# Kernel tuning notes

Hardware: AMD Instinct MI355X
Metric: run time of the kernel (lower is better)

## Reference

```python
import math
import jax, jax.numpy as jnp
import numpy as np

B, S, H, O = 16, 2048, 512, 16


def setup_inputs() -> dict:
    key = jax.random.key(0)
    ks = jax.random.split(key, 8)
    ops = jax.random.normal(ks[7], (S, O), dtype=jnp.float32)
    ops = ops.at[:, 0].set(1.0)  # identity operator (frozen ones)
    return {
        "x": jax.random.normal(ks[0], (B, S, H), dtype=jnp.float32),
        "Wv": jax.random.normal(ks[1], (H, H), dtype=jnp.float32) * 0.02,
        "bv": jax.random.normal(ks[2], (H,), dtype=jnp.float32) * 0.02,
        "Wk": jax.random.normal(ks[3], (H, H), dtype=jnp.float32) * 0.02,
        "bk": jax.random.normal(ks[4], (H,), dtype=jnp.float32) * 0.02,
        "Wq_op": jax.random.normal(ks[5], (H, S), dtype=jnp.float32) * 0.02,
        "bq_op": jax.random.normal(ks[6], (H,), dtype=jnp.float32) * 0.02,
        "operators": ops,
    }


def reference(x, Wv, bv, Wk, bk, Wq_op, bq_op, operators):
    # operator_queries[o] = Linear(S->H)(operator_o)  -> [O, H]
    operator_queries = jnp.einsum('so,hs->oh', operators, Wq_op) + bq_op

    values = x @ Wv.T + bv          # [B, S, H]
    keys = x @ Wk.T + bk            # [B, S, H]

    # single shared key-query logits (original computes it twice identically)
    logits = jnp.einsum('bsh,oh->bso', keys, operator_queries) / math.sqrt(H)

    # relevance softmax over sequence positions s
    relevance_weights = jax.nn.softmax(logits, axis=1)  # [B, S, O]

    # per-operator weighted reduce over s, fused: [B, O, H]
    operator_outputs = jnp.einsum('bsh,bso,so->boh', values, relevance_weights, operators)

    # operator-mixing softmax over operators o
    operator_weights = jax.nn.softmax(logits, axis=-1)  # [B, S, O]

    output = jnp.einsum('bso,boh->bsh', operator_weights, operator_outputs)
    return output, operator_queries
```

## Files before the change

### kernel.cpp

```cpp
#include <hip/hip_runtime.h>

#define BB 16
#define SS 2048
#define HH 512
#define ON 16
#define INV_SQRT_H 0.04419417382415922f

#define WKO_OFF 0
#define C_OFF   8192
#define L_OFF   8208
#define TT_OFF  8464
#define G_OFF   8720
#define OO_OFF  139792
#define ZERO_N  270864
#define OQT_OFF 270864
#define LG_OFF  279056
#define WVT_OFF 803344

__global__ __launch_bounds__(256) void k_oq(const float* __restrict__ Wq,
                                            const float* __restrict__ bq,
                                            const float* __restrict__ ops,
                                            float* __restrict__ ws,
                                            float* __restrict__ oq_out) {
  const int h = blockIdx.x;
  const int t = threadIdx.x;
  float4 acc[4];
  #pragma unroll
  for (int m = 0; m < 4; ++m) acc[m] = make_float4(0.f, 0.f, 0.f, 0.f);
  for (int s = t; s < SS; s += 256) {
    float wq = Wq[(size_t)h * SS + s];
    const float4* op4 = reinterpret_cast<const float4*>(ops + (size_t)s * ON);
    #pragma unroll
    for (int m = 0; m < 4; ++m) {
      float4 v = op4[m];
      acc[m].x += wq * v.x; acc[m].y += wq * v.y;
      acc[m].z += wq * v.z; acc[m].w += wq * v.w;
    }
  }
  __shared__ float red[256][ON];
  #pragma unroll
  for (int m = 0; m < 4; ++m) {
    red[t][4*m+0] = acc[m].x; red[t][4*m+1] = acc[m].y;
    red[t][4*m+2] = acc[m].z; red[t][4*m+3] = acc[m].w;
  }
  __syncthreads();
  for (int st = 128; st > 0; st >>= 1) {
    if (t < st) {
      #pragma unroll
      for (int o = 0; o < ON; ++o) red[t][o] += red[t + st][o];
    }
    __syncthreads();
  }
  if (t < ON) {
    float v = red[0][t] + bq[h];
    oq_out[(size_t)t * HH + h] = v;
    ws[OQT_OFF + (size_t)h * ON + t] = v;
  }
}

__global__ __launch_bounds__(256) void k_wko(const float* __restrict__ Wk,
                                             const float* __restrict__ bk,
                                             float* __restrict__ ws) {
  const int o = blockIdx.x;
  const int hc = blockIdx.y;
  const int t = threadIdx.x;
  const float* __restrict__ oqT = ws + OQT_OFF;
  const int h0 = hc * 64;
  float acc0 = 0.f, acc1 = 0.f;
  for (int h = h0; h < h0 + 64; ++h) {
    float q = oqT[(size_t)h * ON + o];
    acc0 += q * Wk[(size_t)h * HH + t];
    acc1 += q * Wk[(size_t)h * HH + t + 256];
  }
  unsafeAtomicAdd(&ws[WKO_OFF + (size_t)o * HH + t], acc0);
  unsafeAtomicAdd(&ws[WKO_OFF + (size_t)o * HH + t + 256], acc1);
  if (t == 0) {
    float cp = 0.f;
    for (int h = h0; h < h0 + 64; ++h) cp += bk[h] * oqT[(size_t)h * ON + o];
    unsafeAtomicAdd(&ws[C_OFF + o], cp);
  }
}

__global__ __launch_bounds__(256) void k_wvt(const float* __restrict__ Wv,
                                             float* __restrict__ ws) {
  __shared__ float tile[32][33];
  const int tx = threadIdx.x, ty = threadIdx.y;
  const int x0 = blockIdx.x * 32, y0 = blockIdx.y * 32;
  #pragma unroll
  for (int j = 0; j < 4; ++j)
    tile[ty + 8 * j][tx] = Wv[(size_t)(y0 + ty + 8 * j) * HH + x0 + tx];
  __syncthreads();
  float* WvT = ws + WVT_OFF;
  #pragma unroll
  for (int j = 0; j < 4; ++j)
    WvT[(size_t)(x0 + ty + 8 * j) * HH + y0 + tx] = tile[tx][ty + 8 * j];
}

__global__ __launch_bounds__(256) void k_main(const float* __restrict__ x,
                                              const float* __restrict__ ops,
                                              float* __restrict__ ws) {
  const int b = blockIdx.x, sc = blockIdx.y, t = threadIdx.x;
  const int sbase = sc * 64;
  const size_t xbase = ((size_t)b * SS + sbase) * HH;

  __shared__ float red[64][17];
  __shared__ float part[3][64][17];
  __shared__ float el[64][ON];

  const int kq = t >> 6, lane = t & 63;
  const int rg = lane >> 2, oq = lane & 3;
  const int k0 = kq * 128;

  float acc[4][4];
  #pragma unroll
  for (int i = 0; i < 4; ++i)
    #pragma unroll
    for (int j = 0; j < 4; ++j) acc[i][j] = 0.f;

  const float4* __restrict__ wko4 = reinterpret_cast<const float4*>(ws + WKO_OFF);
  #pragma unroll 4
  for (int ch = 0; ch < 32; ++ch) {
    const int kk = k0 + ch * 4;
    float4 xr[4], wr[4];
    #pragma unroll
    for (int i = 0; i < 4; ++i)
      xr[i] = *reinterpret_cast<const float4*>(x + xbase + (size_t)(rg + 16 * i) * HH + kk);
    #pragma unroll
    for (int j = 0; j < 4; ++j)
      wr[j] = wko4[(4 * oq + j) * 128 + (kk >> 2)];
    #pragma unroll
    for (int i = 0; i < 4; ++i)
      #pragma unroll
      for (int j = 0; j < 4; ++j)
        acc[i][j] += xr[i].x * wr[j].x + xr[i].y * wr[j].y
                   + xr[i].z * wr[j].z + xr[i].w * wr[j].w;
  }
  if (kq == 0) {
    #pragma unroll
    for (int i = 0; i < 4; ++i)
      #pragma unroll
      for (int j = 0; j < 4; ++j) red[rg + 16 * i][4 * oq + j] = acc[i][j];
  } else {
    #pragma unroll
    for (int i = 0; i < 4; ++i)
      #pragma unroll
      for (int j = 0; j < 4; ++j) part[kq - 1][rg + 16 * i][4 * oq + j] = acc[i][j];
  }
  __syncthreads();

  {
    const int r = t >> 2, o4 = (t & 3) * 4;
    float lgv[4];
    #pragma unroll
    for (int j = 0; j < 4; ++j) {
      const int o = o4 + j;
      float s = red[r][o] + part[0][r][o] + part[1][r][o] + part[2][r][o] + ws[C_OFF + o];
      lgv[j] = s * INV_SQRT_H;
    }
    *reinterpret_cast<float4*>(ws + LG_OFF + ((size_t)b * SS + sbase + r) * ON + o4) =
        make_float4(lgv[0], lgv[1], lgv[2], lgv[3]);
    *reinterpret_cast<float4*>(&el[r][o4]) =
        make_float4(__expf(lgv[0]), __expf(lgv[1]), __expf(lgv[2]), __expf(lgv[3]));
  }
  __syncthreads();

  if (t < ON) {
    float sl = 0.f, st = 0.f;
    for (int r = 0; r < 64; ++r) {
      float e = el[r][t];
      sl += e;
      st += e * ops[(size_t)(sbase + r) * ON + t];
    }
    unsafeAtomicAdd(&ws[L_OFF + b * ON + t], sl);
    unsafeAtomicAdd(&ws[TT_OFF + b * ON + t], st);
  }

  float a0[ON], a1[ON];
  #pragma unroll
  for (int o = 0; o < ON; ++o) { a0[o] = 0.f; a1[o] = 0.f; }
  for (int s = 0; s < 64; ++s) {
    const float xv0 = x[xbase + (size_t)s * HH + t];
    const float xv1 = x[xbase + (size_t)s * HH + t + 256];
    const float4* e4 = reinterpret_cast<const float4*>(&el[s][0]);
    #pragma unroll
    for (int g = 0; g < 4; ++g) {
      float4 e = e4[g];
      a0[4*g+0] += e.x * xv0; a1[4*g+0] += e.x * xv1;
      a0[4*g+1] += e.y * xv0; a1[4*g+1] += e.y * xv1;
      a0[4*g+2] += e.z * xv0; a1[4*g+2] += e.z * xv1;
      a0[4*g+3] += e.w * xv0; a1[4*g+3] += e.w * xv1;
    }
  }
  float* G = ws + G_OFF + (size_t)b * ON * HH;
  #pragma unroll
  for (int o = 0; o < ON; ++o) {
    unsafeAtomicAdd(&G[(size_t)o * HH + t], a0[o]);
    unsafeAtomicAdd(&G[(size_t)o * HH + t + 256], a1[o]);
  }
}

__global__ __launch_bounds__(256) void k_oo(const float* __restrict__ bv,
                                            float* __restrict__ ws) {
  const int b = blockIdx.x, oqi = blockIdx.y, kq = blockIdx.z, t = threadIdx.x;
  const int o0 = oqi * 4, k0 = kq * 128;
  __shared__ float Gs[4][128];
  __shared__ float invLs[4], tts[4];
  if (t < 4) {
    float invL = 1.f / ws[L_OFF + b * ON + o0 + t];
    invLs[t] = invL;
    tts[t] = ws[TT_OFF + b * ON + o0 + t] * invL;
  }
  __syncthreads();
  {
    int idx = t;
    #pragma unroll
    for (int p = 0; p < 2; ++p, idx += 256) {
      int oo = idx >> 7, kk = idx & 127;
      Gs[oo][kk] = ws[G_OFF + ((size_t)b * ON + o0 + oo) * HH + k0 + kk] * invLs[oo];
    }
  }
  __syncthreads();
  const float* __restrict__ WvT = ws + WVT_OFF;
  float acc[4][2];
  #pragma unroll
  for (int o = 0; o < 4; ++o) { acc[o][0] = 0.f; acc[o][1] = 0.f; }
  for (int k = 0; k < 128; ++k) {
    const float w0 = WvT[(size_t)(k0 + k) * HH + t];
    const float w1 = WvT[(size_t)(k0 + k) * HH + t + 256];
    #pragma unroll
    for (int o = 0; o < 4; ++o) {
      const float g = Gs[o][k];
      acc[o][0] += g * w0; acc[o][1] += g * w1;
    }
  }
  float* OOp = ws + OO_OFF + ((size_t)b * ON + o0) * HH;
  #pragma unroll
  for (int o = 0; o < 4; ++o) {
    float add0 = acc[o][0], add1 = acc[o][1];
    if (kq == 0) { add0 += bv[t] * tts[o]; add1 += bv[t + 256] * tts[o]; }
    unsafeAtomicAdd(&OOp[(size_t)o * HH + t], add0);
    unsafeAtomicAdd(&OOp[(size_t)o * HH + t + 256], add1);
  }
}

__global__ __launch_bounds__(256) void k_out(float* __restrict__ ws,
                                             float* __restrict__ out) {
  const int b = blockIdx.x, sc = blockIdx.y, t = threadIdx.x;
  const int rbase = b * SS + sc * 128;
  __shared__ float OOs[ON * HH];
  __shared__ float wl[128 * ON];
  const float4* OO4 = reinterpret_cast<const float4*>(ws + OO_OFF + (size_t)(b * ON) * HH);
  float4* OOs4 = reinterpret_cast<float4*>(OOs);
  #pragma unroll
  for (int j = 0; j < 8; ++j) OOs4[t + 256 * j] = OO4[t + 256 * j];
  if (t < 128) {
    const float4* lg4 = reinterpret_cast<const float4*>(ws + LG_OFF + (size_t)(rbase + t) * ON);
    float l[ON];
    float4 p0 = lg4[0], p1 = lg4[1], p2 = lg4[2], p3 = lg4[3];
    l[0]=p0.x; l[1]=p0.y; l[2]=p0.z; l[3]=p0.w;
    l[4]=p1.x; l[5]=p1.y; l[6]=p1.z; l[7]=p1.w;
    l[8]=p2.x; l[9]=p2.y; l[10]=p2.z; l[11]=p2.w;
    l[12]=p3.x; l[13]=p3.y; l[14]=p3.z; l[15]=p3.w;
    float m = l[0];
    #pragma unroll
    for (int o = 1; o < ON; ++o) m = fmaxf(m, l[o]);
    float sum = 0.f;
    #pragma unroll
    for (int o = 0; o < ON; ++o) { l[o] = __expf(l[o] - m); sum += l[o]; }
    float inv = 1.f / sum;
    #pragma unroll
    for (int o = 0; o < ON; ++o) wl[t * ON + o] = l[o] * inv;
  }
  __syncthreads();
  const int rsub = t >> 7, hq = t & 127;
  float oo[ON][4];
  #pragma unroll
  for (int o = 0; o < ON; ++o)
    #pragma unroll
    for (int j = 0; j < 4; ++j) oo[o][j] = OOs[o * HH + hq + 128 * j];
  const float4* wl4 = reinterpret_cast<const float4*>(wl);
  for (int i = 0; i < 64; ++i) {
    const int r = rsub * 64 + i;
    float4 w0 = wl4[r * 4 + 0], w1 = wl4[r * 4 + 1], w2 = wl4[r * 4 + 2], w3 = wl4[r * 4 + 3];
    float w[ON];
    w[0]=w0.x; w[1]=w0.y; w[2]=w0.z; w[3]=w0.w;
    w[4]=w1.x; w[5]=w1.y; w[6]=w1.z; w[7]=w1.w;
    w[8]=w2.x; w[9]=w2.y; w[10]=w2.z; w[11]=w2.w;
    w[12]=w3.x; w[13]=w3.y; w[14]=w3.z; w[15]=w3.w;
    float* orow = out + (size_t)(rbase + r) * HH + hq;
    #pragma unroll
    for (int j = 0; j < 4; ++j) {
      float v = 0.f;
      #pragma unroll
      for (int o = 0; o < ON; ++o) v += w[o] * oo[o][j];
      orow[128 * j] = v;
    }
  }
}

extern "C" void kernel_launch(void* const* d_in, const int* in_sizes, int n_in,
                              void* d_out, int out_size, void* d_ws, size_t ws_size,
                              hipStream_t stream) {
  const float* x   = (const float*)d_in[0];
  const float* Wv  = (const float*)d_in[1];
  const float* bv  = (const float*)d_in[2];
  const float* Wk  = (const float*)d_in[3];
  const float* bk  = (const float*)d_in[4];
  const float* Wq  = (const float*)d_in[5];
  const float* bq  = (const float*)d_in[6];
  const float* ops = (const float*)d_in[7];
  float* out = (float*)d_out;
  float* ws  = (float*)d_ws;
  float* oq_out = out + (size_t)BB * SS * HH;

  hipMemsetAsync(ws, 0, (size_t)ZERO_N * sizeof(float), stream);

  k_wvt<<<dim3(16, 16), dim3(32, 8), 0, stream>>>(Wv, ws);
  k_oq<<<512, 256, 0, stream>>>(Wq, bq, ops, ws, oq_out);
  k_wko<<<dim3(16, 8), 256, 0, stream>>>(Wk, bk, ws);
  k_main<<<dim3(16, 32), 256, 0, stream>>>(x, ops, ws);
  k_oo<<<dim3(16, 4, 4), 256, 0, stream>>>(bv, ws);
  k_out<<<dim3(16, 16), 256, 0, stream>>>(ws, out);
}
```

Baseline: 207.6 us.

## Halve row tiles, drop Wv transpose kernel, and vectorize output stage

```diff
diff --git a/kernel.cpp b/kernel.cpp
--- a/kernel.cpp
+++ b/kernel.cpp
@@ -11,11 +11,10 @@
 #define L_OFF   8208
 #define TT_OFF  8464
 #define G_OFF   8720
+#define ZERO_N  139792
 #define OO_OFF  139792
-#define ZERO_N  270864
 #define OQT_OFF 270864
 #define LG_OFF  279056
-#define WVT_OFF 803344
 
 __global__ __launch_bounds__(256) void k_oq(const float* __restrict__ Wq,
                                             const float* __restrict__ bq,
@@ -81,39 +80,24 @@
   }
 }
 
-__global__ __launch_bounds__(256) void k_wvt(const float* __restrict__ Wv,
-                                             float* __restrict__ ws) {
-  __shared__ float tile[32][33];
-  const int tx = threadIdx.x, ty = threadIdx.y;
-  const int x0 = blockIdx.x * 32, y0 = blockIdx.y * 32;
-  #pragma unroll
-  for (int j = 0; j < 4; ++j)
-    tile[ty + 8 * j][tx] = Wv[(size_t)(y0 + ty + 8 * j) * HH + x0 + tx];
-  __syncthreads();
-  float* WvT = ws + WVT_OFF;
-  #pragma unroll
-  for (int j = 0; j < 4; ++j)
-    WvT[(size_t)(x0 + ty + 8 * j) * HH + y0 + tx] = tile[tx][ty + 8 * j];
-}
-
 __global__ __launch_bounds__(256) void k_main(const float* __restrict__ x,
                                               const float* __restrict__ ops,
                                               float* __restrict__ ws) {
   const int b = blockIdx.x, sc = blockIdx.y, t = threadIdx.x;
-  const int sbase = sc * 64;
+  const int sbase = sc * 32;
   const size_t xbase = ((size_t)b * SS + sbase) * HH;
 
-  __shared__ float red[64][17];
-  __shared__ float part[3][64][17];
-  __shared__ float el[64][ON];
+  __shared__ float red[32][17];
+  __shared__ float part[3][32][17];
+  __shared__ float el[32][ON];
 
   const int kq = t >> 6, lane = t & 63;
   const int rg = lane >> 2, oq = lane & 3;
   const int k0 = kq * 128;
 
-  float acc[4][4];
-  #pragma unroll
-  for (int i = 0; i < 4; ++i)
+  float acc[2][4];
+  #pragma unroll
+  for (int i = 0; i < 2; ++i)
     #pragma unroll
     for (int j = 0; j < 4; ++j) acc[i][j] = 0.f;
 
@@ -121,15 +105,15 @@
   #pragma unroll 4
   for (int ch = 0; ch < 32; ++ch) {
     const int kk = k0 + ch * 4;
-    float4 xr[4], wr[4];
-    #pragma unroll
-    for (int i = 0; i < 4; ++i)
+    float4 xr[2], wr[4];
+    #pragma unroll
+    for (int i = 0; i < 2; ++i)
       xr[i] = *reinterpret_cast<const float4*>(x + xbase + (size_t)(rg + 16 * i) * HH + kk);
     #pragma unroll
     for (int j = 0; j < 4; ++j)
       wr[j] = wko4[(4 * oq + j) * 128 + (kk >> 2)];
     #pragma unroll
-    for (int i = 0; i < 4; ++i)
+    for (int i = 0; i < 2; ++i)
       #pragma unroll
       for (int j = 0; j < 4; ++j)
         acc[i][j] += xr[i].x * wr[j].x + xr[i].y * wr[j].y
@@ -137,18 +121,18 @@
   }
   if (kq == 0) {
     #pragma unroll
-    for (int i = 0; i < 4; ++i)
+    for (int i = 0; i < 2; ++i)
       #pragma unroll
       for (int j = 0; j < 4; ++j) red[rg + 16 * i][4 * oq + j] = acc[i][j];
   } else {
     #pragma unroll
-    for (int i = 0; i < 4; ++i)
+    for (int i = 0; i < 2; ++i)
       #pragma unroll
       for (int j = 0; j < 4; ++j) part[kq - 1][rg + 16 * i][4 * oq + j] = acc[i][j];
   }
   __syncthreads();
 
-  {
+  if (t < 128) {
     const int r = t >> 2, o4 = (t & 3) * 4;
     float lgv[4];
     #pragma unroll
@@ -166,7 +150,7 @@
 
   if (t < ON) {
     float sl = 0.f, st = 0.f;
-    for (int r = 0; r < 64; ++r) {
+    for (int r = 0; r < 32; ++r) {
       float e = el[r][t];
       sl += e;
       st += e * ops[(size_t)(sbase + r) * ON + t];
@@ -178,7 +162,7 @@
   float a0[ON], a1[ON];
   #pragma unroll
   for (int o = 0; o < ON; ++o) { a0[o] = 0.f; a1[o] = 0.f; }
-  for (int s = 0; s < 64; ++s) {
+  for (int s = 0; s < 32; ++s) {
     const float xv0 = x[xbase + (size_t)s * HH + t];
     const float xv1 = x[xbase + (size_t)s * HH + t + 256];
     const float4* e4 = reinterpret_cast<const float4*>(&el[s][0]);
@@ -199,11 +183,12 @@
   }
 }
 
-__global__ __launch_bounds__(256) void k_oo(const float* __restrict__ bv,
+__global__ __launch_bounds__(256) void k_oo(const float* __restrict__ Wv,
+                                            const float* __restrict__ bv,
                                             float* __restrict__ ws) {
-  const int b = blockIdx.x, oqi = blockIdx.y, kq = blockIdx.z, t = threadIdx.x;
-  const int o0 = oqi * 4, k0 = kq * 128;
-  __shared__ float Gs[4][128];
+  const int b = blockIdx.x, oqi = blockIdx.y, hqi = blockIdx.z, t = threadIdx.x;
+  const int o0 = oqi * 4, h0 = hqi * 128;
+  __shared__ float4 Gs[4][128];
   __shared__ float invLs[4], tts[4];
   if (t < 4) {
     float invL = 1.f / ws[L_OFF + b * ON + o0 + t];
@@ -216,44 +201,43 @@
     #pragma unroll
     for (int p = 0; p < 2; ++p, idx += 256) {
       int oo = idx >> 7, kk = idx & 127;
-      Gs[oo][kk] = ws[G_OFF + ((size_t)b * ON + o0 + oo) * HH + k0 + kk] * invLs[oo];
-    }
-  }
-  __syncthreads();
-  const float* __restrict__ WvT = ws + WVT_OFF;
-  float acc[4][2];
-  #pragma unroll
-  for (int o = 0; o < 4; ++o) { acc[o][0] = 0.f; acc[o][1] = 0.f; }
-  for (int k = 0; k < 128; ++k) {
-    const float w0 = WvT[(size_t)(k0 + k) * HH + t];
-    const float w1 = WvT[(size_t)(k0 + k) * HH + t + 256];
-    #pragma unroll
-    for (int o = 0; o < 4; ++o) {
-      const float g = Gs[o][k];
-      acc[o][0] += g * w0; acc[o][1] += g * w1;
-    }
+      float4 g = reinterpret_cast<const float4*>(
+          ws + G_OFF + ((size_t)b * ON + o0 + oo) * HH)[kk];
+      float sv = invLs[oo];
+      Gs[oo][kk] = make_float4(g.x * sv, g.y * sv, g.z * sv, g.w * sv);
+    }
+  }
+  __syncthreads();
+  const int hh = h0 + (t & 127);
+  const int op = (t >> 7) * 2;
+  const float4* __restrict__ wv4 = reinterpret_cast<const float4*>(Wv + (size_t)hh * HH);
+  float a0 = 0.f, a1 = 0.f;
+  #pragma unroll 4
+  for (int kk = 0; kk < 128; ++kk) {
+    float4 wv = wv4[kk];
+    float4 g0 = Gs[op][kk], g1 = Gs[op + 1][kk];
+    a0 += g0.x * wv.x + g0.y * wv.y + g0.z * wv.z + g0.w * wv.w;
+    a1 += g1.x * wv.x + g1.y * wv.y + g1.z * wv.z + g1.w * wv.w;
   }
   float* OOp = ws + OO_OFF + ((size_t)b * ON + o0) * HH;
-  #pragma unroll
-  for (int o = 0; o < 4; ++o) {
-    float add0 = acc[o][0], add1 = acc[o][1];
-    if (kq == 0) { add0 += bv[t] * tts[o]; add1 += bv[t + 256] * tts[o]; }
-    unsafeAtomicAdd(&OOp[(size_t)o * HH + t], add0);
-    unsafeAtomicAdd(&OOp[(size_t)o * HH + t + 256], add1);
-  }
+  OOp[(size_t)op * HH + hh]       = a0 + bv[hh] * tts[op];
+  OOp[(size_t)(op + 1) * HH + hh] = a1 + bv[hh] * tts[op + 1];
 }
 
 __global__ __launch_bounds__(256) void k_out(float* __restrict__ ws,
                                              float* __restrict__ out) {
   const int b = blockIdx.x, sc = blockIdx.y, t = threadIdx.x;
-  const int rbase = b * SS + sc * 128;
-  __shared__ float OOs[ON * HH];
-  __shared__ float wl[128 * ON];
-  const float4* OO4 = reinterpret_cast<const float4*>(ws + OO_OFF + (size_t)(b * ON) * HH);
-  float4* OOs4 = reinterpret_cast<float4*>(OOs);
-  #pragma unroll
-  for (int j = 0; j < 8; ++j) OOs4[t + 256 * j] = OO4[t + 256 * j];
-  if (t < 128) {
+  const int rbase = b * SS + sc * 32;
+  __shared__ float wl[32 * ON];
+
+  float4 oo4[ON];
+  const float4* __restrict__ OO4 =
+      reinterpret_cast<const float4*>(ws + OO_OFF + (size_t)b * ON * HH);
+  const int hq = t & 127;
+  #pragma unroll
+  for (int o = 0; o < ON; ++o) oo4[o] = OO4[o * 128 + hq];
+
+  if (t < 32) {
     const float4* lg4 = reinterpret_cast<const float4*>(ws + LG_OFF + (size_t)(rbase + t) * ON);
     float l[ON];
     float4 p0 = lg4[0], p1 = lg4[1], p2 = lg4[2], p3 = lg4[3];
@@ -272,29 +256,25 @@
     for (int o = 0; o < ON; ++o) wl[t * ON + o] = l[o] * inv;
   }
   __syncthreads();
-  const int rsub = t >> 7, hq = t & 127;
-  float oo[ON][4];
-  #pragma unroll
-  for (int o = 0; o < ON; ++o)
-    #pragma unroll
-    for (int j = 0; j < 4; ++j) oo[o][j] = OOs[o * HH + hq + 128 * j];
+
+  const int rsub = t >> 7;
   const float4* wl4 = reinterpret_cast<const float4*>(wl);
-  for (int i = 0; i < 64; ++i) {
-    const int r = rsub * 64 + i;
+  float4* __restrict__ out4 = reinterpret_cast<float4*>(out);
+  for (int i = 0; i < 16; ++i) {
+    const int r = rsub * 16 + i;
     float4 w0 = wl4[r * 4 + 0], w1 = wl4[r * 4 + 1], w2 = wl4[r * 4 + 2], w3 = wl4[r * 4 + 3];
     float w[ON];
     w[0]=w0.x; w[1]=w0.y; w[2]=w0.z; w[3]=w0.w;
     w[4]=w1.x; w[5]=w1.y; w[6]=w1.z; w[7]=w1.w;
     w[8]=w2.x; w[9]=w2.y; w[10]=w2.z; w[11]=w2.w;
     w[12]=w3.x; w[13]=w3.y; w[14]=w3.z; w[15]=w3.w;
-    float* orow = out + (size_t)(rbase + r) * HH + hq;
-    #pragma unroll
-    for (int j = 0; j < 4; ++j) {
-      float v = 0.f;
-      #pragma unroll
-      for (int o = 0; o < ON; ++o) v += w[o] * oo[o][j];
-      orow[128 * j] = v;
-    }
+    float4 v = make_float4(0.f, 0.f, 0.f, 0.f);
+    #pragma unroll
+    for (int o = 0; o < ON; ++o) {
+      v.x += w[o] * oo4[o].x; v.y += w[o] * oo4[o].y;
+      v.z += w[o] * oo4[o].z; v.w += w[o] * oo4[o].w;
+    }
+    out4[(size_t)(rbase + r) * 128 + hq] = v;
   }
 }
 
@@ -315,10 +295,9 @@
 
   hipMemsetAsync(ws, 0, (size_t)ZERO_N * sizeof(float), stream);
 
-  k_wvt<<<dim3(16, 16), dim3(32, 8), 0, stream>>>(Wv, ws);
   k_oq<<<512, 256, 0, stream>>>(Wq, bq, ops, ws, oq_out);
   k_wko<<<dim3(16, 8), 256, 0, stream>>>(Wk, bk, ws);
-  k_main<<<dim3(16, 32), 256, 0, stream>>>(x, ops, ws);
-  k_oo<<<dim3(16, 4, 4), 256, 0, stream>>>(bv, ws);
-  k_out<<<dim3(16, 16), 256, 0, stream>>>(ws, out);
-}
+  k_main<<<dim3(16, 64), 256, 0, stream>>>(x, ops, ws);
+  k_oo<<<dim3(16, 4, 4), 256, 0, stream>>>(Wv, bv, ws);
+  k_out<<<dim3(16, 64), 256, 0, stream>>>(ws, out);
+}
```

Result: slower. 245.1 us (+18.1%).
